# Kernel optimization log

Measured on AMD Instinct MI355X. Metric: run time of the kernel, lower is better.

The kernel has to match this reference:

```python
import jax, jax.numpy as jnp
import numpy as np

SEARCH_RANGE = 2  # matches init_kwargs


def setup_inputs() -> dict:
    key = jax.random.key(0)
    k1, k2 = jax.random.split(key)
    B, C, H, W = 8, 128, 160, 160
    c1 = jax.random.normal(k1, (B, C, H, W), dtype=jnp.float32)
    c2_backwarped = jax.random.normal(k2, (B, C, H, W), dtype=jnp.float32)
    prelu_weight = jnp.full((1,), 0.25, dtype=jnp.float32)  # nn.PReLU default init
    return {"c1": c1, "c2_backwarped": c2_backwarped, "prelu_weight": prelu_weight}


def reference(c1, c2_backwarped, prelu_weight):
    r = SEARCH_RANGE
    max_offset = 2 * r + 1
    h, w = c1.shape[-2:]
    # reflect-pad spatial dims of the warped feature map
    padded = jnp.pad(c2_backwarped, ((0, 0), (0, 0), (r, r), (r, r)), mode="reflect")
    inv_c = 1.0 / c1.shape[1]
    costs = []
    for y in range(max_offset):  # small fixed 5x5 offset loop
        for x in range(max_offset):
            sl = padded[:, :, y:y + h, x:x + w]          # [B,C,H,W]
            costs.append(jnp.sum(c1 * sl, axis=1) * inv_c)  # channel mean -> [B,H,W]
    cv = jnp.stack(costs, axis=1)  # [B, 25, H, W]
    # PReLU with a single shared slope parameter
    a = prelu_weight[0]
    return jnp.where(cv >= 0, cv, a * cv)
```

## Files before the change

### kernel.cpp

```cpp
#include <hip/hip_runtime.h>

#define BATCH 8
#define CHN 128
#define HH 160
#define WW 160
#define HW (HH*WW)
#define RR 2
#define MAXOFF 5
#define NOFF 25
#define TW 32
#define TH 8
#define PW (TW + 2*RR)
#define PH (TH + 2*RR)
#define NG 4
#define CPG (CHN/NG)
#define RC 2
#define SCH (NG*RC)
#define ROUNDS (CPG/RC)
#define NPT 64
#define NTHREADS 256
#define CHFL (PH*PW)
#define STFL (SCH*CHFL)
#define NSLOT 14
#define OCH 4

__device__ __forceinline__ int reflect_idx(int i, int n) {
    if (i < 0) i = -i;
    if (i >= n) i = 2 * (n - 1) - i;
    return i;
}

__global__ __launch_bounds__(NTHREADS) void costvol_kernel(
    const float* __restrict__ c1,
    const float* __restrict__ c2,
    const float* __restrict__ pw,
    float* __restrict__ out)
{
    __shared__ float lds[STFL];

    const int tid = threadIdx.x;
    const int g  = tid >> 6;
    const int pt = tid & (NPT - 1);
    const int xh = pt & 15;
    const int yg = pt >> 4;

    int bidx = (int)blockIdx.x;
    bidx = (bidx & 7) * 100 + (bidx >> 3);
    const int tx0 = (bidx % (WW / TW)) * TW; bidx /= (WW / TW);
    const int ty0 = (bidx % (HH / TH)) * TH; bidx /= (HH / TH);
    const int b = bidx;

    int boff[NSLOT];
#pragma unroll
    for (int k = 0; k < NSLOT; ++k) {
        const int idx = tid + k * NTHREADS;
        if (idx < STFL) {
            int c   = idx / CHFL;
            int rem = idx - c * CHFL;
            int ty  = rem / PW;
            int tx  = rem - ty * PW;
            int gh  = c >> 1, j = c & 1;
            int gr  = reflect_idx(ty0 - RR + ty, HH);
            int gc  = reflect_idx(tx0 - RR + tx, WW);
            boff[k] = ((gh * CPG + j) * HW + gr * WW + gc) * 4;
        } else {
            boff[k] = 0;
        }
    }

    const char*  c2b = (const char*)(c2 + (size_t)b * CHN * HW);
    const float* c1p = c1 + ((size_t)b * CHN + g * CPG) * HW
                          + (ty0 + 2 * yg) * WW + tx0 + xh * 2;

    float  sv[NSLOT];
    float2 sc0[RC], sc1[RC], sn0[RC], sn1[RC];

    auto issue_c2 = [&](int r) {
        const char* base = c2b + (size_t)r * RC * HW * 4;
#pragma unroll
        for (int k = 0; k < NSLOT; ++k)
            if (tid + k * NTHREADS < STFL)
                sv[k] = *(const float*)(base + boff[k]);
    };
    auto write_lds = [&]() {
#pragma unroll
        for (int k = 0; k < NSLOT; ++k)
            if (tid + k * NTHREADS < STFL)
                lds[tid + k * NTHREADS] = sv[k];
    };
    auto issue_c1 = [&](int r, float2* d0, float2* d1) {
#pragma unroll
        for (int j = 0; j < RC; ++j) {
            d0[j] = *(const float2*)(c1p + (size_t)(r * RC + j) * HW);
            d1[j] = *(const float2*)(c1p + (size_t)(r * RC + j) * HW + WW);
        }
    };

    float2 acc0[NOFF], acc1[NOFF];
#pragma unroll
    for (int i = 0; i < NOFF; ++i) {
        acc0[i] = make_float2(0.f, 0.f);
        acc1[i] = make_float2(0.f, 0.f);
    }

    issue_c2(0);
    issue_c1(0, sc0, sc1);
    write_lds();
    __syncthreads();
    issue_c2(1);
    issue_c1(1, sn0, sn1);

    for (int r = 0; r < ROUNDS; ++r) {
        const float* lbase = lds + (g * RC) * CHFL + (2 * yg) * PW + xh * 2;
#pragma unroll
        for (int j = 0; j < RC; ++j) {
            const float* tb = lbase + j * CHFL;
            float2 wr[6][3];
#pragma unroll
            for (int dr = 0; dr < 6; ++dr) {
                wr[dr][0] = *(const float2*)(tb + dr * PW);
                wr[dr][1] = *(const float2*)(tb + dr * PW + 2);
                wr[dr][2] = *(const float2*)(tb + dr * PW + 4);
            }
            const float2 s0 = sc0[j];
            const float2 s1 = sc1[j];
#pragma unroll
            for (int dy = 0; dy < MAXOFF; ++dy) {
                {
                    const float2 w0 = wr[dy][0], w1 = wr[dy][1], w2 = wr[dy][2];
                    float2* A = &acc0[dy * MAXOFF];
                    A[0].x = fmaf(s0.x, w0.x, A[0].x);  A[0].y = fmaf(s0.y, w0.y, A[0].y);
                    A[1].x = fmaf(s0.x, w0.y, A[1].x);  A[1].y = fmaf(s0.y, w1.x, A[1].y);
                    A[2].x = fmaf(s0.x, w1.x, A[2].x);  A[2].y = fmaf(s0.y, w1.y, A[2].y);
                    A[3].x = fmaf(s0.x, w1.y, A[3].x);  A[3].y = fmaf(s0.y, w2.x, A[3].y);
                    A[4].x = fmaf(s0.x, w2.x, A[4].x);  A[4].y = fmaf(s0.y, w2.y, A[4].y);
                }
                {
                    const float2 w0 = wr[dy + 1][0], w1 = wr[dy + 1][1], w2 = wr[dy + 1][2];
                    float2* A = &acc1[dy * MAXOFF];
                    A[0].x = fmaf(s1.x, w0.x, A[0].x);  A[0].y = fmaf(s1.y, w0.y, A[0].y);
                    A[1].x = fmaf(s1.x, w0.y, A[1].x);  A[1].y = fmaf(s1.y, w1.x, A[1].y);
                    A[2].x = fmaf(s1.x, w1.x, A[2].x);  A[2].y = fmaf(s1.y, w1.y, A[2].y);
                    A[3].x = fmaf(s1.x, w1.y, A[3].x);  A[3].y = fmaf(s1.y, w2.x, A[3].y);
                    A[4].x = fmaf(s1.x, w2.x, A[4].x);  A[4].y = fmaf(s1.y, w2.y, A[4].y);
                }
            }
        }
        __syncthreads();
        if (r + 1 < ROUNDS) {
            write_lds();
#pragma unroll
            for (int j = 0; j < RC; ++j) {
                sc0[j] = sn0[j];
                sc1[j] = sn1[j];
            }
            __syncthreads();
            if (r + 2 < ROUNDS) {
                issue_c2(r + 2);
                issue_c1(r + 2, sn0, sn1);
            }
        }
    }

    const float a = pw[0];
    const float inv_c = 1.0f / (float)CHN;
    float2* e0 = (float2*)lds;
    float2* e1 = (float2*)(lds + 3 * OCH * NPT * 2);

    for (int o0 = 0; o0 < NOFF; o0 += OCH) {
        const int K = (NOFF - o0) < OCH ? (NOFF - o0) : OCH;
        __syncthreads();
        if (g > 0) {
#pragma unroll
            for (int k = 0; k < OCH; ++k)
                if (k < K) {
                    e0[((g - 1) * OCH + k) * NPT + pt] = acc0[o0 + k];
                    e1[((g - 1) * OCH + k) * NPT + pt] = acc1[o0 + k];
                }
        }
        __syncthreads();
        if (g == 0) {
#pragma unroll
            for (int k = 0; k < OCH; ++k) {
                if (k < K) {
                    const int o = o0 + k;
                    float2 u = acc0[o];
                    float2 v = acc1[o];
#pragma unroll
                    for (int q = 0; q < 3; ++q) {
                        float2 ua = e0[(q * OCH + k) * NPT + pt];
                        float2 va = e1[(q * OCH + k) * NPT + pt];
                        u.x += ua.x; u.y += ua.y;
                        v.x += va.x; v.y += va.y;
                    }
                    float ux = u.x * inv_c, uy = u.y * inv_c;
                    float vx = v.x * inv_c, vy = v.y * inv_c;
                    ux = (ux >= 0.f) ? ux : a * ux;
                    uy = (uy >= 0.f) ? uy : a * uy;
                    vx = (vx >= 0.f) ? vx : a * vx;
                    vy = (vy >= 0.f) ? vy : a * vy;
                    float* op = out + (size_t)(b * NOFF + o) * HW
                              + (ty0 + 2 * yg) * WW + tx0 + xh * 2;
                    *(float2*)op        = make_float2(ux, uy);
                    *(float2*)(op + WW) = make_float2(vx, vy);
                }
            }
        }
    }
}

extern "C" void kernel_launch(void* const* d_in, const int* in_sizes, int n_in,
                              void* d_out, int out_size, void* d_ws, size_t ws_size,
                              hipStream_t stream) {
    const float* c1 = (const float*)d_in[0];
    const float* c2 = (const float*)d_in[1];
    const float* pw = (const float*)d_in[2];
    float* out = (float*)d_out;

    dim3 grid((WW / TW) * (HH / TH) * BATCH);
    dim3 block(NTHREADS);
    costvol_kernel<<<grid, block, 0, stream>>>(c1, c2, pw, out);
}
```

Measured before the change: 54.46 us.

## Give each wavefront a private LDS slice to drop block-wide barriers in main loop

Each 64-thread wavefront now loads the c2 halo tile for its own channel group into a private LDS slice, so the two __syncthreads per round in the channel loop are removed. Wave-internal ordering stands in for the barriers between LDS writes and reads. The cost is that each wave issues all of its own halo loads instead of sharing the load across the block. Correctness relies on lockstep execution within a wave and on LDS ordering from the compiler's waitcnt handling, with no explicit wave barrier.

```diff
diff --git a/kernel.cpp b/kernel.cpp
--- a/kernel.cpp
+++ b/kernel.cpp
@@ -15,13 +15,13 @@
 #define NG 4
 #define CPG (CHN/NG)
 #define RC 2
-#define SCH (NG*RC)
 #define ROUNDS (CPG/RC)
-#define NPT 64
 #define NTHREADS 256
 #define CHFL (PH*PW)
-#define STFL (SCH*CHFL)
+#define WSLICE (RC*CHFL)
+#define STFL (NG*WSLICE)
 #define NSLOT 14
+#define NPT 64
 #define OCH 4
 
 __device__ __forceinline__ int reflect_idx(int i, int n) {
@@ -38,11 +38,11 @@
 {
     __shared__ float lds[STFL];
 
-    const int tid = threadIdx.x;
-    const int g  = tid >> 6;
-    const int pt = tid & (NPT - 1);
-    const int xh = pt & 15;
-    const int yg = pt >> 4;
+    const int tid  = threadIdx.x;
+    const int g    = tid >> 6;
+    const int lane = tid & 63;
+    const int xh   = lane & 15;
+    const int yg   = lane >> 4;
 
     int bidx = (int)blockIdx.x;
     bidx = (bidx & 7) * 100 + (bidx >> 3);
@@ -53,24 +53,24 @@
     int boff[NSLOT];
 #pragma unroll
     for (int k = 0; k < NSLOT; ++k) {
-        const int idx = tid + k * NTHREADS;
-        if (idx < STFL) {
-            int c   = idx / CHFL;
-            int rem = idx - c * CHFL;
+        const int idx = lane + k * 64;
+        if (idx < WSLICE) {
+            int j   = idx / CHFL;
+            int rem = idx - j * CHFL;
             int ty  = rem / PW;
             int tx  = rem - ty * PW;
-            int gh  = c >> 1, j = c & 1;
             int gr  = reflect_idx(ty0 - RR + ty, HH);
             int gc  = reflect_idx(tx0 - RR + tx, WW);
-            boff[k] = ((gh * CPG + j) * HW + gr * WW + gc) * 4;
+            boff[k] = ((g * CPG + j) * HW + gr * WW + gc) * 4;
         } else {
             boff[k] = 0;
         }
     }
 
-    const char*  c2b = (const char*)(c2 + (size_t)b * CHN * HW);
-    const float* c1p = c1 + ((size_t)b * CHN + g * CPG) * HW
-                          + (ty0 + 2 * yg) * WW + tx0 + xh * 2;
+    const char*  c2b  = (const char*)(c2 + (size_t)b * CHN * HW);
+    const float* c1p  = c1 + ((size_t)b * CHN + g * CPG) * HW
+                           + (ty0 + 2 * yg) * WW + tx0 + xh * 2;
+    float* const  sl  = lds + g * WSLICE;
 
     float  sv[NSLOT];
     float2 sc0[RC], sc1[RC], sn0[RC], sn1[RC];
@@ -79,14 +79,14 @@
         const char* base = c2b + (size_t)r * RC * HW * 4;
 #pragma unroll
         for (int k = 0; k < NSLOT; ++k)
-            if (tid + k * NTHREADS < STFL)
+            if (lane + k * 64 < WSLICE)
                 sv[k] = *(const float*)(base + boff[k]);
     };
-    auto write_lds = [&]() {
+    auto write_slice = [&]() {
 #pragma unroll
         for (int k = 0; k < NSLOT; ++k)
-            if (tid + k * NTHREADS < STFL)
-                lds[tid + k * NTHREADS] = sv[k];
+            if (lane + k * 64 < WSLICE)
+                sl[lane + k * 64] = sv[k];
     };
     auto issue_c1 = [&](int r, float2* d0, float2* d1) {
 #pragma unroll
@@ -105,13 +105,12 @@
 
     issue_c2(0);
     issue_c1(0, sc0, sc1);
-    write_lds();
-    __syncthreads();
+    write_slice();
     issue_c2(1);
     issue_c1(1, sn0, sn1);
 
     for (int r = 0; r < ROUNDS; ++r) {
-        const float* lbase = lds + (g * RC) * CHFL + (2 * yg) * PW + xh * 2;
+        const float* lbase = sl + (2 * yg) * PW + xh * 2;
 #pragma unroll
         for (int j = 0; j < RC; ++j) {
             const float* tb = lbase + j * CHFL;
@@ -146,15 +145,13 @@
                 }
             }
         }
-        __syncthreads();
         if (r + 1 < ROUNDS) {
-            write_lds();
+            write_slice();
 #pragma unroll
             for (int j = 0; j < RC; ++j) {
                 sc0[j] = sn0[j];
                 sc1[j] = sn1[j];
             }
-            __syncthreads();
             if (r + 2 < ROUNDS) {
                 issue_c2(r + 2);
                 issue_c1(r + 2, sn0, sn1);
@@ -165,17 +162,18 @@
     const float a = pw[0];
     const float inv_c = 1.0f / (float)CHN;
     float2* e0 = (float2*)lds;
-    float2* e1 = (float2*)(lds + 3 * OCH * NPT * 2);
+    float2* e1 = e0 + (NG - 1) * OCH * NPT;
+
+    __syncthreads();
 
     for (int o0 = 0; o0 < NOFF; o0 += OCH) {
         const int K = (NOFF - o0) < OCH ? (NOFF - o0) : OCH;
-        __syncthreads();
         if (g > 0) {
 #pragma unroll
             for (int k = 0; k < OCH; ++k)
                 if (k < K) {
-                    e0[((g - 1) * OCH + k) * NPT + pt] = acc0[o0 + k];
-                    e1[((g - 1) * OCH + k) * NPT + pt] = acc1[o0 + k];
+                    e0[((g - 1) * OCH + k) * NPT + lane] = acc0[o0 + k];
+                    e1[((g - 1) * OCH + k) * NPT + lane] = acc1[o0 + k];
                 }
         }
         __syncthreads();
@@ -187,9 +185,9 @@
                     float2 u = acc0[o];
                     float2 v = acc1[o];
 #pragma unroll
-                    for (int q = 0; q < 3; ++q) {
-                        float2 ua = e0[(q * OCH + k) * NPT + pt];
-                        float2 va = e1[(q * OCH + k) * NPT + pt];
+                    for (int q = 0; q < NG - 1; ++q) {
+                        float2 ua = e0[(q * OCH + k) * NPT + lane];
+                        float2 va = e1[(q * OCH + k) * NPT + lane];
                         u.x += ua.x; u.y += ua.y;
                         v.x += va.x; v.y += va.y;
                     }
@@ -206,6 +204,8 @@
                 }
             }
         }
+        if (o0 + OCH < NOFF)
+            __syncthreads();
     }
 }
 
```

New measurement: 69.33 us. 1.27x slower.
